# Kernel tuning notes

Measured on AMD Instinct MI355X. Metric: run time of the kernel, lower is better.

Reference implementation:

```python
import jax, jax.numpy as jnp
import numpy as np

W_BITS = 8
A_BITS = 8


def sym_quant(x, num_bits):
    # Symmetric per-last-dim abs-max quantization (SymQuantizer.forward, ndim<=3,
    # layerwise=False): s = (2^(b-1)-1)/(max|x| + 1e-6); q = round(x*s)/(s+1e-6)
    max_abs = jnp.max(jnp.abs(x), axis=-1, keepdims=True)
    s = (2.0 ** (num_bits - 1) - 1.0) / (max_abs + 1e-6)
    return jnp.round(x * s) / (s + 1e-6)


def setup_inputs() -> dict:
    key = jax.random.key(0)
    kx, kw = jax.random.split(key)
    B, S, NX, NF = 4, 2048, 1600, 6400
    x = jax.random.normal(kx, (B, S, NX), dtype=jnp.float32)
    weight = 0.02 * jax.random.normal(kw, (NX, NF), dtype=jnp.float32)  # Conv1D: [nx, nf]
    bias = jnp.zeros((NF,), dtype=jnp.float32)
    return {"x": x, "weight": weight, "bias": bias}


def reference(x, weight, bias):
    # quantize weights per-row (over nf), quantize activations per-token (over nx)
    wq = sym_quant(weight, W_BITS)
    xq = sym_quant(x, A_BITS)
    # addmm(bias, x.view(-1, nx), weight) then reshape back
    return jnp.einsum("bsx,xf->bsf", xq, wq) + bias
```

## Files before the change

kernel.cpp:

```cpp
#include <hip/hip_runtime.h>
#include <stdint.h>

typedef _Float16 f16;
typedef _Float16 f16x4 __attribute__((ext_vector_type(4)));
typedef _Float16 f16x8 __attribute__((ext_vector_type(8)));
typedef float f32x4 __attribute__((ext_vector_type(4)));

#define K_DIM 1600
#define NF_DIM 6400
#define KPAD 1664
#define NKT 26
#define KPB (KPAD * 2)

#define BUFSZ 57344
#define BOFF 16384

__device__ __forceinline__ void async_copy16(const void* g, void* l) {
    __builtin_amdgcn_global_load_lds(
        (const __attribute__((address_space(1))) void*)(uintptr_t)g,
        (__attribute__((address_space(3))) void*)(uint32_t)(uintptr_t)l,
        16, 0, 0);
}

__device__ __forceinline__ float blockMax(float v, float* sm) {
#pragma unroll
    for (int off = 32; off > 0; off >>= 1)
        v = fmaxf(v, __shfl_down(v, off, 64));
    int wid = threadIdx.x >> 6, lane = threadIdx.x & 63;
    if (lane == 0) sm[wid] = v;
    __syncthreads();
    if (threadIdx.x == 0) {
        float m = sm[0];
        for (int i = 1; i < (int)(blockDim.x >> 6); ++i) m = fmaxf(m, sm[i]);
        sm[0] = m;
    }
    __syncthreads();
    return sm[0];
}

__global__ void quant_x_kernel(const float* __restrict__ x, f16* __restrict__ qx,
                               float* __restrict__ ax) {
    __shared__ float sm[4];
    size_t row = blockIdx.x;
    const float* xr = x + row * (size_t)K_DIM;
    float m = 0.f;
    const int n4 = K_DIM >> 2;
    for (int i = threadIdx.x; i < n4; i += blockDim.x) {
        float4 v = ((const float4*)xr)[i];
        m = fmaxf(fmaxf(fmaxf(fabsf(v.x), fabsf(v.y)), fmaxf(fabsf(v.z), fabsf(v.w))), m);
    }
    m = blockMax(m, sm);
    float s = 127.0f / (m + 1e-6f);
    if (threadIdx.x == 0) ax[row] = 1.0f / (s + 1e-6f);
    f16* qr = qx + row * (size_t)KPAD;
    for (int i = threadIdx.x; i < n4; i += blockDim.x) {
        float4 v = ((const float4*)xr)[i];
        f16x4 q;
        q[0] = (f16)rintf(v.x * s);
        q[1] = (f16)rintf(v.y * s);
        q[2] = (f16)rintf(v.z * s);
        q[3] = (f16)rintf(v.w * s);
        *(f16x4*)&qr[i * 4] = q;
    }
    if (threadIdx.x < 16) {
        f16x4 z = {};
        *(f16x4*)&qr[K_DIM + threadIdx.x * 4] = z;
    }
}

__global__ void wscale_kernel(const float* __restrict__ w, float* __restrict__ sw) {
    __shared__ float sm[4];
    size_t k = blockIdx.x;
    const float* wr = w + k * (size_t)NF_DIM;
    float m = 0.f;
    const int n4 = NF_DIM >> 2;
    for (int i = threadIdx.x; i < n4; i += blockDim.x) {
        float4 v = ((const float4*)wr)[i];
        m = fmaxf(fmaxf(fmaxf(fabsf(v.x), fabsf(v.y)), fmaxf(fabsf(v.z), fabsf(v.w))), m);
    }
    m = blockMax(m, sm);
    if (threadIdx.x == 0) sw[k] = 127.0f / (m + 1e-6f);
}

__global__ void wtq_kernel(const float* __restrict__ w, const float* __restrict__ sw,
                           f16* __restrict__ wqt) {
    __shared__ f16 t[64][80];
    int k0 = blockIdx.x * 64;
    int f0 = blockIdx.y * 64;
    int tid = threadIdx.x;
    if (k0 >= K_DIM) {
        int fr = tid >> 2;
        int ch = (tid & 3) << 4;
        float4 z = {};
        float4* dst = (float4*)&wqt[(size_t)(f0 + fr) * KPAD + k0 + ch];
        dst[0] = z;
        dst[1] = z;
        return;
    }
    int rr = tid >> 4;
    int cc = (tid & 15) << 2;
#pragma unroll
    for (int i = 0; i < 4; ++i) {
        int r = rr + i * 16;
        float s = sw[k0 + r];
        float inv = 1.0f / (s + 1e-6f);
        float4 v = *(const float4*)&w[(size_t)(k0 + r) * NF_DIM + f0 + cc];
        t[cc + 0][r] = (f16)(rintf(v.x * s) * inv);
        t[cc + 1][r] = (f16)(rintf(v.y * s) * inv);
        t[cc + 2][r] = (f16)(rintf(v.z * s) * inv);
        t[cc + 3][r] = (f16)(rintf(v.w * s) * inv);
    }
    __syncthreads();
    int fr = tid >> 2;
    int ch = (tid & 3) << 4;
    const float4* src = (const float4*)&t[fr][ch];
    float4* dst = (float4*)&wqt[(size_t)(f0 + fr) * KPAD + k0 + ch];
    dst[0] = src[0];
    dst[1] = src[1];
}

__global__ __launch_bounds__(512, 1) void gemm128x320(
    const f16* __restrict__ A,
    const f16* __restrict__ Bt,
    const float* __restrict__ ax,
    const float* __restrict__ bias,
    float* __restrict__ C, int M, int N) {
    extern __shared__ char lds[];

    const int tid = threadIdx.x;
    const int lane = tid & 63;
    const int wv = tid >> 6;
    const int wm = wv >> 2;
    const int wn = wv & 3;
    const int lr = lane & 15;
    const int lg = lane >> 4;

    const int bid = blockIdx.x;
    const int cpx = gridDim.x >> 3;
    const int swz = (bid & 7) * cpx + (bid >> 3);
    const int tm = swz & 63;
    const int tn = swz >> 6;
    const size_t m0 = (size_t)tm * 128, n0 = (size_t)tn * 320;

    const int srow8 = lane >> 3;
    const int sslot = (lane & 7) ^ srow8;
    const char* pA = (const char*)A + (m0 + (size_t)(wv * 8 + srow8)) * KPB + sslot * 16;
    const char* pB = (const char*)Bt + (n0 + (size_t)(wv * 8 + srow8)) * KPB + sslot * 16;
    const int L0 = wv * 1024 + lane * 16;

#define ST_A(bufo, t)                                                          \
    {                                                                          \
        const char* g_ = pA + (size_t)(t) * 128;                               \
        async_copy16(g_, lds + (bufo) + L0);                                   \
        async_copy16(g_ + (size_t)64 * KPB, lds + (bufo) + 8192 + L0);         \
    }
#define ST_B(bufo, t)                                                          \
    {                                                                          \
        const char* g_ = pB + (size_t)(t) * 128;                               \
        _Pragma("unroll") for (int c_ = 0; c_ < 5; ++c_)                       \
            async_copy16(g_ + (size_t)(c_ * 64) * KPB,                         \
                         lds + (bufo) + BOFF + c_ * 8192 + L0);                \
    }

    const int swz0 = ((lg) ^ (lr & 7)) << 4;
    const int swz1 = ((4 + lg) ^ (lr & 7)) << 4;
    const int rbA = (wm * 64 + lr) * 128;
    const int rbB = BOFF + wn * 10240 + lr * 128;

#define RD_A(dst, bufo, rowoff, sz)                                    \
    {                                                                  \
        const char* p_ = lds + (bufo) + rbA + (rowoff) + (sz);         \
        dst[0] = *(const f16x8*)(p_);                                  \
        dst[1] = *(const f16x8*)(p_ + 2048);                           \
    }
#define RD_B(dst, bufo, sz)                                            \
    {                                                                  \
        const char* p_ = lds + (bufo) + rbB + (sz);                    \
        _Pragma("unroll") for (int n_ = 0; n_ < 5; ++n_)               \
            dst[n_] = *(const f16x8*)(p_ + n_ * 2048);                 \
    }

#define BARRIER __builtin_amdgcn_s_barrier()
#define LGKM(n) asm volatile("s_waitcnt lgkmcnt(" #n ")" ::: "memory")
#define VM5 asm volatile("s_waitcnt vmcnt(5)" ::: "memory")
#define SB0 __builtin_amdgcn_sched_barrier(0)

#define MF25(AF, BF, R0)                                                          \
    {                                                                             \
        __builtin_amdgcn_s_setprio(1);                                            \
        _Pragma("unroll") for (int a_ = 0; a_ < 2; ++a_)                          \
        _Pragma("unroll") for (int n_ = 0; n_ < 5; ++n_)                          \
            acc[(R0) + a_][n_] = __builtin_amdgcn_mfma_f32_16x16x32_f16(          \
                AF[a_], BF[n_], acc[(R0) + a_][n_], 0, 0, 0);                     \
        __builtin_amdgcn_s_setprio(0);                                            \
    }

#define TILE(CUR, NXT, tn2)                                           \
    {                                                                 \
                                                             \
        RD_A(aN, CUR, 0, swz1);                                       \
        RD_B(B1, CUR, swz1);                                          \
        LGKM(7); SB0;                                                 \
        MF25(aP, B0, 0);                                              \
                                                             \
        RD_A(aP, CUR, 4096, swz0);                                    \
        LGKM(2); SB0;                                                 \
        MF25(aN, B1, 0);                                              \
        BARRIER;              \
                              \
        ST_B(CUR, tn2);                                               \
        RD_A(aN, CUR, 4096, swz1);                                    \
        LGKM(2); SB0;                                                 \
        MF25(aP, B0, 2);                                              \
                                                             \
        LGKM(0);                 \
        VM5; SB0;           \
        BARRIER;                    \
        ST_A(CUR, tn2);                                               \
        RD_A(aP, NXT, 0, swz0);                                       \
        RD_B(B0, NXT, swz0);                                          \
        SB0;                                                          \
        MF25(aN, B1, 2);                                              \
    }

    f32x4 acc[4][5] = {};
    f16x8 aP[2], aN[2], B0[5], B1[5];

    ST_A(0, 0);
    ST_B(0, 0);
    ST_A(BUFSZ, 1);
    ST_B(BUFSZ, 1);
    asm volatile("s_waitcnt vmcnt(7)" ::: "memory");
    BARRIER;
    RD_A(aP, 0, 0, swz0);
    RD_B(B0, 0, swz0);

    for (int i = 0; i < NKT; i += 2) {
        const int ta = (i + 2 < NKT) ? i + 2 : NKT - 1;
        const int tb = (i + 3 < NKT) ? i + 3 : NKT - 1;
        TILE(0, BUFSZ, ta);
        TILE(BUFSZ, 0, tb);
    }
    asm volatile("s_waitcnt vmcnt(0) lgkmcnt(0)" ::: "memory");

    float bv[5];
#pragma unroll
    for (int n_ = 0; n_ < 5; ++n_) bv[n_] = bias[n0 + wn * 80 + n_ * 16 + lr];
#pragma unroll
    for (int a = 0; a < 4; ++a) {
#pragma unroll
        for (int j = 0; j < 4; ++j) {
            size_t row = m0 + wm * 64 + a * 16 + lg * 4 + j;
            float axv = ax[row];
            float* crow = C + row * (size_t)N + n0 + wn * 80;
#pragma unroll
            for (int n_ = 0; n_ < 5; ++n_)
                crow[n_ * 16 + lr] = acc[a][n_][j] * axv + bv[n_];
        }
    }
}

extern "C" void kernel_launch(void* const* d_in, const int* in_sizes, int n_in,
                              void* d_out, int out_size, void* d_ws, size_t ws_size,
                              hipStream_t stream) {
    const float* x = (const float*)d_in[0];
    const float* w = (const float*)d_in[1];
    const float* bias = (const float*)d_in[2];
    float* out = (float*)d_out;

    const int M = in_sizes[0] / K_DIM;
    const int N = NF_DIM;

    char* ws = (char*)d_ws;
    f16* qx = (f16*)ws;
    f16* wqt = (f16*)(ws + (size_t)M * KPAD * 2);
    float* ax = (float*)(ws + (size_t)M * KPAD * 2 + (size_t)N * KPAD * 2);
    float* sw = ax + M;

    quant_x_kernel<<<M, 256, 0, stream>>>(x, qx, ax);
    wscale_kernel<<<K_DIM, 256, 0, stream>>>(w, sw);
    wtq_kernel<<<dim3(KPAD / 64, NF_DIM / 64), 256, 0, stream>>>(w, sw, wqt);

    (void)hipFuncSetAttribute((const void*)gemm128x320,
                              hipFuncAttributeMaxDynamicSharedMemorySize, 2 * BUFSZ);
    gemm128x320<<<(M / 128) * (N / 320), 512, 2 * BUFSZ, stream>>>(qx, wqt, ax, bias, out, M, N);
}
```

Measured before the change: 222.3 us.

## Enlarge GEMM block tile to 256x320 with restructured double-buffer pipeline

```diff
diff --git a/kernel.cpp b/kernel.cpp
--- a/kernel.cpp
+++ b/kernel.cpp
@@ -12,8 +12,10 @@
 #define NKT 26
 #define KPB (KPAD * 2)
 
-#define BUFSZ 57344
-#define BOFF 16384
+#define ABYTES 32768
+#define BBYTES 40960
+#define BUFSZ (ABYTES + BBYTES)
+#define BOFF ABYTES
 
 __device__ __forceinline__ void async_copy16(const void* g, void* l) {
     __builtin_amdgcn_global_load_lds(
@@ -119,7 +121,7 @@
     dst[1] = src[1];
 }
 
-__global__ __launch_bounds__(512, 1) void gemm128x320(
+__global__ __launch_bounds__(512, 1) void gemm256x320(
     const f16* __restrict__ A,
     const f16* __restrict__ Bt,
     const float* __restrict__ ax,
@@ -138,54 +140,69 @@
     const int bid = blockIdx.x;
     const int cpx = gridDim.x >> 3;
     const int swz = (bid & 7) * cpx + (bid >> 3);
-    const int tm = swz & 63;
-    const int tn = swz >> 6;
-    const size_t m0 = (size_t)tm * 128, n0 = (size_t)tn * 320;
+    const int tm = swz & 31;
+    const int tn = swz >> 5;
+    const size_t m0 = (size_t)tm * 256, n0 = (size_t)tn * 320;
 
     const int srow8 = lane >> 3;
     const int sslot = (lane & 7) ^ srow8;
-    const char* pA = (const char*)A + (m0 + (size_t)(wv * 8 + srow8)) * KPB + sslot * 16;
-    const char* pB = (const char*)Bt + (n0 + (size_t)(wv * 8 + srow8)) * KPB + sslot * 16;
-    const int L0 = wv * 1024 + lane * 16;
+    const char* pA = (const char*)A + (m0 + (size_t)(wv * 32 + srow8)) * KPB + sslot * 16;
+    const char* pB = (const char*)Bt + (n0 + (size_t)(wv * 40 + srow8)) * KPB + sslot * 16;
+    const int LA0 = wv * 4096 + lane * 16;
+    const int LB0 = BOFF + wv * 5120 + lane * 16;
 
 #define ST_A(bufo, t)                                                          \
     {                                                                          \
         const char* g_ = pA + (size_t)(t) * 128;                               \
-        async_copy16(g_, lds + (bufo) + L0);                                   \
-        async_copy16(g_ + (size_t)64 * KPB, lds + (bufo) + 8192 + L0);         \
+        _Pragma("unroll") for (int j_ = 0; j_ < 4; ++j_)                       \
+            async_copy16(g_ + (size_t)(j_ * 8) * KPB,                          \
+                         lds + (bufo) + LA0 + j_ * 1024);                      \
     }
 #define ST_B(bufo, t)                                                          \
     {                                                                          \
         const char* g_ = pB + (size_t)(t) * 128;                               \
         _Pragma("unroll") for (int c_ = 0; c_ < 5; ++c_)                       \
-            async_copy16(g_ + (size_t)(c_ * 64) * KPB,                         \
-                         lds + (bufo) + BOFF + c_ * 8192 + L0);                \
-    }
-
-    const int swz0 = ((lg) ^ (lr & 7)) << 4;
-    const int swz1 = ((4 + lg) ^ (lr & 7)) << 4;
-    const int rbA = (wm * 64 + lr) * 128;
-    const int rbB = BOFF + wn * 10240 + lr * 128;
-
-#define RD_A(dst, bufo, rowoff, sz)                                    \
+            async_copy16(g_ + (size_t)(c_ * 8) * KPB,                          \
+                         lds + (bufo) + LB0 + c_ * 1024);                      \
+    }
+
+    const int adr0 = (wm * 128 + lr) * 128 + ((((lg)) ^ (lr & 7)) << 4);
+    const int adr1 = (wm * 128 + lr) * 128 + (((4 + lg) ^ (lr & 7)) << 4);
+    const int bdr0 = BOFF + (wn * 80 + lr) * 128 + (((lg) ^ (lr & 7)) << 4);
+    const int bdr1 = BOFF + (wn * 80 + lr) * 128 + (((4 + lg) ^ (lr & 7)) << 4);
+
+#define RD_P(dst, bufo, p, AOFF)                                       \
     {                                                                  \
-        const char* p_ = lds + (bufo) + rbA + (rowoff) + (sz);         \
+        const char* p_ = lds + (bufo) + (AOFF) + (p) * 4096;           \
         dst[0] = *(const f16x8*)(p_);                                  \
         dst[1] = *(const f16x8*)(p_ + 2048);                           \
     }
-#define RD_B(dst, bufo, sz)                                            \
+#define RD_B5(dst, bufo, BOFFK)                                        \
     {                                                                  \
-        const char* p_ = lds + (bufo) + rbB + (sz);                    \
+        const char* p_ = lds + (bufo) + (BOFFK);                       \
         _Pragma("unroll") for (int n_ = 0; n_ < 5; ++n_)               \
             dst[n_] = *(const f16x8*)(p_ + n_ * 2048);                 \
     }
+#define RD_B01(dst, bufo, BOFFK)                                       \
+    {                                                                  \
+        const char* p_ = lds + (bufo) + (BOFFK);                       \
+        dst[0] = *(const f16x8*)(p_);                                  \
+        dst[1] = *(const f16x8*)(p_ + 2048);                           \
+    }
+#define RD_B234(dst, bufo, BOFFK)                                      \
+    {                                                                  \
+        const char* p_ = lds + (bufo) + (BOFFK);                       \
+        dst[2] = *(const f16x8*)(p_ + 2 * 2048);                       \
+        dst[3] = *(const f16x8*)(p_ + 3 * 2048);                       \
+        dst[4] = *(const f16x8*)(p_ + 4 * 2048);                       \
+    }
 
 #define BARRIER __builtin_amdgcn_s_barrier()
 #define LGKM(n) asm volatile("s_waitcnt lgkmcnt(" #n ")" ::: "memory")
-#define VM5 asm volatile("s_waitcnt vmcnt(5)" ::: "memory")
+#define VM0 asm volatile("s_waitcnt vmcnt(0)" ::: "memory")
 #define SB0 __builtin_amdgcn_sched_barrier(0)
 
-#define MF25(AF, BF, R0)                                                          \
+#define MF10(AF, BF, R0)                                                          \
     {                                                                             \
         __builtin_amdgcn_s_setprio(1);                                            \
         _Pragma("unroll") for (int a_ = 0; a_ < 2; ++a_)                          \
@@ -195,49 +212,62 @@
         __builtin_amdgcn_s_setprio(0);                                            \
     }
 
-#define TILE(CUR, NXT, tn2)                                           \
+#define TILE(CUR, NXT, tn1)                                           \
     {                                                                 \
                                                              \
-        RD_A(aN, CUR, 0, swz1);                                       \
-        RD_B(B1, CUR, swz1);                                          \
+        RD_P(aN, CUR, 1, adr0);                                       \
+        RD_B01(Bk1, CUR, bdr1);                                       \
+        ST_A(NXT, tn1);                                               \
+        LGKM(4); SB0;                                                 \
+        MF10(aP, Bk0, 0);                                             \
+                                                             \
+        RD_P(aP, CUR, 2, adr0);                                       \
+        RD_B234(Bk1, CUR, bdr1);                                      \
         LGKM(7); SB0;                                                 \
-        MF25(aP, B0, 0);                                              \
-                                                             \
-        RD_A(aP, CUR, 4096, swz0);                                    \
+        MF10(aN, Bk0, 2);                                             \
+                                                             \
+        RD_P(aN, CUR, 3, adr0);                                       \
+        ST_B(NXT, tn1);                                               \
+        LGKM(5); SB0;                                                 \
+        MF10(aP, Bk0, 4);                                             \
+                                                             \
+        RD_P(aP, CUR, 0, adr1);                                       \
         LGKM(2); SB0;                                                 \
-        MF25(aN, B1, 0);                                              \
-        BARRIER;              \
-                              \
-        ST_B(CUR, tn2);                                               \
-        RD_A(aN, CUR, 4096, swz1);                                    \
+        MF10(aN, Bk0, 6);                                             \
+                                                             \
+        RD_P(aN, CUR, 1, adr1);                                       \
         LGKM(2); SB0;                                                 \
-        MF25(aP, B0, 2);                                              \
-                                                             \
-        LGKM(0);                 \
-        VM5; SB0;           \
-        BARRIER;                    \
-        ST_A(CUR, tn2);                                               \
-        RD_A(aP, NXT, 0, swz0);                                       \
-        RD_B(B0, NXT, swz0);                                          \
+        MF10(aP, Bk1, 0);                                             \
+                                                             \
+        RD_P(aP, CUR, 2, adr1);                                       \
+        LGKM(2); SB0;                                                 \
+        MF10(aN, Bk1, 2);                                             \
+                                                             \
+        RD_P(aN, CUR, 3, adr1);                                       \
+        LGKM(2); SB0;                                                 \
+        MF10(aP, Bk1, 4);                                             \
+                                                             \
+        VM0; LGKM(0); SB0;                                            \
+        BARRIER;                                                      \
+        RD_P(aP, NXT, 0, adr0);                                       \
+        RD_B5(Bk0, NXT, bdr0);                                        \
         SB0;                                                          \
-        MF25(aN, B1, 2);                                              \
-    }
-
-    f32x4 acc[4][5] = {};
-    f16x8 aP[2], aN[2], B0[5], B1[5];
+        MF10(aN, Bk1, 6);                                             \
+    }
+
+    f32x4 acc[8][5] = {};
+    f16x8 aP[2], aN[2], Bk0[5], Bk1[5];
 
     ST_A(0, 0);
     ST_B(0, 0);
-    ST_A(BUFSZ, 1);
-    ST_B(BUFSZ, 1);
-    asm volatile("s_waitcnt vmcnt(7)" ::: "memory");
+    VM0;
     BARRIER;
-    RD_A(aP, 0, 0, swz0);
-    RD_B(B0, 0, swz0);
-
-    for (int i = 0; i < NKT; i += 2) {
-        const int ta = (i + 2 < NKT) ? i + 2 : NKT - 1;
-        const int tb = (i + 3 < NKT) ? i + 3 : NKT - 1;
+    RD_P(aP, 0, 0, adr0);
+    RD_B5(Bk0, 0, bdr0);
+
+    for (int i = 0; i < NKT / 2; ++i) {
+        const int ta = 2 * i + 1;
+        const int tb = (2 * i + 2 < NKT) ? 2 * i + 2 : NKT - 1;
         TILE(0, BUFSZ, ta);
         TILE(BUFSZ, 0, tb);
     }
@@ -247,10 +277,10 @@
 #pragma unroll
     for (int n_ = 0; n_ < 5; ++n_) bv[n_] = bias[n0 + wn * 80 + n_ * 16 + lr];
 #pragma unroll
-    for (int a = 0; a < 4; ++a) {
+    for (int a = 0; a < 8; ++a) {
 #pragma unroll
         for (int j = 0; j < 4; ++j) {
-            size_t row = m0 + wm * 64 + a * 16 + lg * 4 + j;
+            size_t row = m0 + wm * 128 + a * 16 + lg * 4 + j;
             float axv = ax[row];
             float* crow = C + row * (size_t)N + n0 + wn * 80;
 #pragma unroll
@@ -281,7 +311,7 @@
     wscale_kernel<<<K_DIM, 256, 0, stream>>>(w, sw);
     wtq_kernel<<<dim3(KPAD / 64, NF_DIM / 64), 256, 0, stream>>>(w, sw, wqt);
 
-    (void)hipFuncSetAttribute((const void*)gemm128x320,
+    (void)hipFuncSetAttribute((const void*)gemm256x320,
                               hipFuncAttributeMaxDynamicSharedMemorySize, 2 * BUFSZ);
-    gemm128x320<<<(M / 128) * (N / 320), 512, 2 * BUFSZ, stream>>>(qx, wqt, ax, bias, out, M, N);
-}
+    gemm256x320<<<(M / 256) * (N / 320), 512, 2 * BUFSZ, stream>>>(qx, wqt, ax, bias, out, M, N);
+}
```

After: 241.8 us. 8.8% more time.
